# Performance work log

Measured on AMD Instinct MI355X. Metric: run time of the kernel, lower is better.

Reference implementation:

```python
import jax, jax.numpy as jnp
import numpy as np

RATIO = 0.6
ROT_FACTOR = 0.1  # fraction of 2*pi
B, H, W, C = 32, 512, 512, 3
S = 2 * max(H, W)  # mask side = 2*max(H, W) = 1024
FILL_VALUE = 1  # source references undefined self.fill_value; stripes are set to 1


def setup_inputs() -> dict:
    key = jax.random.key(0)
    k1, k2 = jax.random.split(key)
    images = jax.random.uniform(k1, (B, H, W, C), jnp.float32) * 255.0
    max_ang = ROT_FACTOR * 2.0 * np.pi
    angles = jax.random.uniform(k2, (B,), jnp.float32, -max_ang, max_ang)
    rng = np.random.default_rng(0)
    lo = int(min(H * 0.5, W * 0.3))
    hi = int(max(H * 0.5, W * 0.3))
    gridblock = rng.integers(lo, hi + 1, size=B).astype(np.int32)
    start1 = rng.integers(0, gridblock + 1).astype(np.int32)  # uniform [0, gridblock]
    start2 = rng.integers(0, gridblock + 1).astype(np.int32)
    return {
        "images": images,
        "angles": angles,
        "gridblock": jnp.asarray(gridblock),
        "start1": jnp.asarray(start1),
        "start2": jnp.asarray(start2),
    }


def _build_masks(gridblock, start1, start2):
    # Vectorized equivalent of the nested scatter loops: mask[i,j] = 1 iff
    # row i is in a stripe (pass 1) OR column j is in a stripe (pass 2).
    gb = gridblock[:, None].astype(jnp.int32)  # [B,1]
    length = jnp.clip((gb.astype(jnp.float32) * RATIO + 0.5).astype(jnp.int32), 1, gb - 1)
    n = S // gb  # number of stripes per image
    r = jnp.arange(S, dtype=jnp.int32)[None, :]  # [1,S]

    def stripes(start):
        d = r - start[:, None]
        return (d >= 0) & (jnp.mod(d, gb) < length) & ((d // gb) < n)

    rows = stripes(start1)  # [B,S]
    cols = stripes(start2)  # [B,S]
    return (rows[:, :, None] | cols[:, None, :]).astype(jnp.float32)  # [B,S,S]


def _rotate_bilinear_reflect(mask, angles):
    # Rotate each mask about its center by angles[b] (CCW), bilinear interp,
    # reflect fill (TF 'reflect': d c b a | a b c d | d c b a).
    c = (S - 1) / 2.0
    yy, xx = jnp.meshgrid(jnp.arange(S, dtype=jnp.float32),
                          jnp.arange(S, dtype=jnp.float32), indexing="ij")
    cos = jnp.cos(angles)[:, None, None]
    sin = jnp.sin(angles)[:, None, None]
    x = xx[None] - c
    y = yy[None] - c
    sx = cos * x + sin * y + c  # inverse-map source coords [B,S,S]
    sy = -sin * x + cos * y + c
    x0 = jnp.floor(sx)
    y0 = jnp.floor(sy)
    fx = sx - x0
    fy = sy - y0
    x0i = x0.astype(jnp.int32)
    y0i = y0.astype(jnp.int32)

    def refl(i):
        m = jnp.mod(i, 2 * S)
        return jnp.where(m < S, m, 2 * S - 1 - m)

    x0r, x1r = refl(x0i), refl(x0i + 1)
    y0r, y1r = refl(y0i), refl(y0i + 1)
    b = jnp.arange(mask.shape[0])[:, None, None]
    v00 = mask[b, y0r, x0r]
    v01 = mask[b, y0r, x1r]
    v10 = mask[b, y1r, x0r]
    v11 = mask[b, y1r, x1r]
    return (v00 * (1 - fx) * (1 - fy) + v01 * fx * (1 - fy)
            + v10 * (1 - fx) * fy + v11 * fx * fy)


def reference(images, angles, gridblock, start1, start2):
    mask = _build_masks(gridblock, start1, start2) * FILL_VALUE  # [B,S,S]
    rot = _rotate_bilinear_reflect(mask, angles)
    off_h = (S - H) // 2
    off_w = (S - W) // 2
    m = rot[:, off_h:off_h + H, off_w:off_w + W]  # center crop [B,H,W]
    return images * m[..., None]
```

## Files before the change

### kernel.cpp

```cpp
#include <hip/hip_runtime.h>

namespace {
constexpr int S = 1024;
constexpr int H = 512;
constexpr int W = 512;
constexpr int B = 32;
constexpr int OFF = 256;

__device__ __forceinline__ int refl(int i) {
    int m = i & (2 * S - 1);
    return (m < S) ? m : (2 * S - 1 - m);
}

__device__ __forceinline__ bool stripe(int i, int start, int gb, int len, int n, float inv_gb) {
    int d = i - start;
    if (d < 0) return false;
    int q = (int)((float)d * inv_gb);
    int r = d - q * gb;
    if (r < 0)        { r += gb; --q; }
    else if (r >= gb) { r -= gb; ++q; }
    return (r < len) && (q < n);
}

__global__ __launch_bounds__(256) void gridmask_kernel(
    const float* __restrict__ images,
    const float* __restrict__ angles,
    const int* __restrict__ gridblock,
    const int* __restrict__ start1,
    const int* __restrict__ start2,
    float* __restrict__ out)
{
    const int t   = blockIdx.x * 256 + threadIdx.x;
    const int b   = t >> 16;
    const int rem = t & 65535;
    const int y   = rem >> 7;
    const int x   = (rem & 127) << 2;

    const float ang = angles[b];
    const int gb = gridblock[b];
    const int s1 = start1[b];
    const int s2 = start2[b];

    const float gbf = (float)gb;
    int len = (int)(__fadd_rn(__fmul_rn(gbf, 0.6f), 0.5f));
    len = min(max(len, 1), gb - 1);
    const int n = S / gb;
    const float inv_gb = 1.0f / gbf;

    float sn, cs;
    sincosf(ang, &sn, &cs);

    const float c = (float)(S - 1) * 0.5f;
    const float Y = (float)(y + OFF) - c;

    const size_t base = (size_t)t * 12;
    const float4* ip = (const float4*)(images + base);
    const float4 p0 = ip[0];
    const float4 p1 = ip[1];
    const float4 p2 = ip[2];

    float m[4];
#pragma unroll
    for (int i = 0; i < 4; ++i) {
        const float X  = (float)(x + i + OFF) - c;
        const float sx =  cs * X + sn * Y + c;
        const float sy =  cs * Y - sn * X + c;
        const float x0f = floorf(sx);
        const float y0f = floorf(sy);
        const float fx = sx - x0f;
        const float fy = sy - y0f;
        const int x0i = (int)x0f;
        const int y0i = (int)y0f;
        const int x0r = refl(x0i), x1r = refl(x0i + 1);
        const int y0r = refl(y0i), y1r = refl(y0i + 1);
        const bool c0 = stripe(x0r, s2, gb, len, n, inv_gb);
        const bool c1 = stripe(x1r, s2, gb, len, n, inv_gb);
        const bool r0 = stripe(y0r, s1, gb, len, n, inv_gb);
        const bool r1 = stripe(y1r, s1, gb, len, n, inv_gb);
        const float v00 = (r0 | c0) ? 1.0f : 0.0f;
        const float v01 = (r0 | c1) ? 1.0f : 0.0f;
        const float v10 = (r1 | c0) ? 1.0f : 0.0f;
        const float v11 = (r1 | c1) ? 1.0f : 0.0f;
        m[i] = (v00 * (1.0f - fx) + v01 * fx) * (1.0f - fy)
             + (v10 * (1.0f - fx) + v11 * fx) * fy;
    }

    float4 o0, o1, o2;
    o0.x = p0.x * m[0]; o0.y = p0.y * m[0]; o0.z = p0.z * m[0]; o0.w = p0.w * m[1];
    o1.x = p1.x * m[1]; o1.y = p1.y * m[1]; o1.z = p1.z * m[2]; o1.w = p1.w * m[2];
    o2.x = p2.x * m[2]; o2.y = p2.y * m[3]; o2.z = p2.z * m[3]; o2.w = p2.w * m[3];

    float4* op = (float4*)(out + base);
    op[0] = o0; op[1] = o1; op[2] = o2;
}
}

extern "C" void kernel_launch(void* const* d_in, const int* in_sizes, int n_in,
                              void* d_out, int out_size, void* d_ws, size_t ws_size,
                              hipStream_t stream) {
    const float* images    = (const float*)d_in[0];
    const float* angles    = (const float*)d_in[1];
    const int*   gridblock = (const int*)d_in[2];
    const int*   start1    = (const int*)d_in[3];
    const int*   start2    = (const int*)d_in[4];
    float* outp = (float*)d_out;

    const int total_groups = B * H * W / 4;
    const int blocks = total_groups / 256;
    gridmask_kernel<<<blocks, 256, 0, stream>>>(images, angles, gridblock, start1, start2, outp);
}
```

Baseline: 183.7 us.

## Stage mask values in LDS to coalesce image loads and stores

Each block now handles 1024 pixels. It first computes the rotated mask values into shared memory, then reads and writes the image as fully coalesced float4 streams, with consecutive threads touching consecutive float4s. Each thread picks the right mask value from LDS through a divide-by-3 index. Before, each thread loaded 3 strided float4s spaced 48 bytes apart; the new pattern gives contiguous wavefront accesses, at the cost of a barrier and LDS traffic.

```diff
diff --git a/kernel.cpp b/kernel.cpp
--- a/kernel.cpp
+++ b/kernel.cpp
@@ -30,68 +30,93 @@
     const int* __restrict__ start2,
     float* __restrict__ out)
 {
-    const int t   = blockIdx.x * 256 + threadIdx.x;
-    const int b   = t >> 16;
-    const int rem = t & 65535;
-    const int y   = rem >> 7;
-    const int x   = (rem & 127) << 2;
+    __shared__ float mlds[1024];
 
-    const float ang = angles[b];
-    const int gb = gridblock[b];
-    const int s1 = start1[b];
-    const int s2 = start2[b];
+    const int tid = threadIdx.x;
+    const int blk = blockIdx.x;
+    const int b   = blk >> 8;
+    const int pix_base = (blk & 255) << 10;
 
-    const float gbf = (float)gb;
-    int len = (int)(__fadd_rn(__fmul_rn(gbf, 0.6f), 0.5f));
-    len = min(max(len, 1), gb - 1);
-    const int n = S / gb;
-    const float inv_gb = 1.0f / gbf;
+    {
+        const int p0   = tid << 2;
+        const int gpix = pix_base + p0;
+        const int y    = gpix >> 9;
+        const int x    = gpix & 511;
 
-    float sn, cs;
-    sincosf(ang, &sn, &cs);
+        const float ang = angles[b];
+        const int gb = gridblock[b];
+        const int s1 = start1[b];
+        const int s2 = start2[b];
 
-    const float c = (float)(S - 1) * 0.5f;
-    const float Y = (float)(y + OFF) - c;
+        const float gbf = (float)gb;
+        int len = (int)(__fadd_rn(__fmul_rn(gbf, 0.6f), 0.5f));
+        len = min(max(len, 1), gb - 1);
+        const int n = S / gb;
+        const float inv_gb = 1.0f / gbf;
 
-    const size_t base = (size_t)t * 12;
-    const float4* ip = (const float4*)(images + base);
-    const float4 p0 = ip[0];
-    const float4 p1 = ip[1];
-    const float4 p2 = ip[2];
+        float sn, cs;
+        sincosf(ang, &sn, &cs);
 
-    float m[4];
+        const float c = (float)(S - 1) * 0.5f;
+        const float Y = (float)(y + OFF) - c;
+
+        float m[4];
 #pragma unroll
-    for (int i = 0; i < 4; ++i) {
-        const float X  = (float)(x + i + OFF) - c;
-        const float sx =  cs * X + sn * Y + c;
-        const float sy =  cs * Y - sn * X + c;
-        const float x0f = floorf(sx);
-        const float y0f = floorf(sy);
-        const float fx = sx - x0f;
-        const float fy = sy - y0f;
-        const int x0i = (int)x0f;
-        const int y0i = (int)y0f;
-        const int x0r = refl(x0i), x1r = refl(x0i + 1);
-        const int y0r = refl(y0i), y1r = refl(y0i + 1);
-        const bool c0 = stripe(x0r, s2, gb, len, n, inv_gb);
-        const bool c1 = stripe(x1r, s2, gb, len, n, inv_gb);
-        const bool r0 = stripe(y0r, s1, gb, len, n, inv_gb);
-        const bool r1 = stripe(y1r, s1, gb, len, n, inv_gb);
-        const float v00 = (r0 | c0) ? 1.0f : 0.0f;
-        const float v01 = (r0 | c1) ? 1.0f : 0.0f;
-        const float v10 = (r1 | c0) ? 1.0f : 0.0f;
-        const float v11 = (r1 | c1) ? 1.0f : 0.0f;
-        m[i] = (v00 * (1.0f - fx) + v01 * fx) * (1.0f - fy)
-             + (v10 * (1.0f - fx) + v11 * fx) * fy;
+        for (int i = 0; i < 4; ++i) {
+            const float X  = (float)(x + i + OFF) - c;
+            const float sx =  cs * X + sn * Y + c;
+            const float sy =  cs * Y - sn * X + c;
+            const float x0f = floorf(sx);
+            const float y0f = floorf(sy);
+            const float fx = sx - x0f;
+            const float fy = sy - y0f;
+            const int x0i = (int)x0f;
+            const int y0i = (int)y0f;
+            const int x0r = refl(x0i), x1r = refl(x0i + 1);
+            const int y0r = refl(y0i), y1r = refl(y0i + 1);
+            const bool c0 = stripe(x0r, s2, gb, len, n, inv_gb);
+            const bool c1 = stripe(x1r, s2, gb, len, n, inv_gb);
+            const bool r0 = stripe(y0r, s1, gb, len, n, inv_gb);
+            const bool r1 = stripe(y1r, s1, gb, len, n, inv_gb);
+            const float v00 = (r0 | c0) ? 1.0f : 0.0f;
+            const float v01 = (r0 | c1) ? 1.0f : 0.0f;
+            const float v10 = (r1 | c0) ? 1.0f : 0.0f;
+            const float v11 = (r1 | c1) ? 1.0f : 0.0f;
+            m[i] = (v00 * (1.0f - fx) + v01 * fx) * (1.0f - fy)
+                 + (v10 * (1.0f - fx) + v11 * fx) * fy;
+        }
+        float4* ml4 = (float4*)mlds;
+        ml4[tid] = make_float4(m[0], m[1], m[2], m[3]);
     }
+    __syncthreads();
 
-    float4 o0, o1, o2;
-    o0.x = p0.x * m[0]; o0.y = p0.y * m[0]; o0.z = p0.z * m[0]; o0.w = p0.w * m[1];
-    o1.x = p1.x * m[1]; o1.y = p1.y * m[1]; o1.z = p1.z * m[2]; o1.w = p1.w * m[2];
-    o2.x = p2.x * m[2]; o2.y = p2.y * m[3]; o2.z = p2.z * m[3]; o2.w = p2.w * m[3];
+    const size_t fbase = (size_t)blk * 3072;
+    const float4* __restrict__ gin4  = (const float4*)(images + fbase);
+    float4* __restrict__       gout4 = (float4*)(out + fbase);
 
-    float4* op = (float4*)(out + base);
-    op[0] = o0; op[1] = o1; op[2] = o2;
+    const float4 p0 = gin4[tid];
+    const float4 p1 = gin4[tid + 256];
+    const float4 p2 = gin4[tid + 512];
+
+#pragma unroll
+    for (int j = 0; j < 3; ++j) {
+        const int lf = (j << 10) + (tid << 2);
+        const int q  = lf / 3;
+        const int r  = lf - q * 3;
+        const float ma = mlds[q];
+        const float mb = mlds[q + 1 <= 1023 ? q + 1 : 1023];
+        const float m0 = (r + 0 >= 3) ? mb : ma;
+        const float m1 = (r + 1 >= 3) ? mb : ma;
+        const float m2 = (r + 2 >= 3) ? mb : ma;
+        const float m3 = (r + 3 >= 3) ? mb : ma;
+        const float4 p = (j == 0) ? p0 : (j == 1) ? p1 : p2;
+        float4 o;
+        o.x = p.x * m0;
+        o.y = p.y * m1;
+        o.z = p.z * m2;
+        o.w = p.w * m3;
+        gout4[(j << 8) + tid] = o;
+    }
 }
 }
 
@@ -105,7 +130,6 @@
     const int*   start2    = (const int*)d_in[4];
     float* outp = (float*)d_out;
 
-    const int total_groups = B * H * W / 4;
-    const int blocks = total_groups / 256;
+    const int blocks = B * H * W / 1024;
     gridmask_kernel<<<blocks, 256, 0, stream>>>(images, angles, gridblock, start1, start2, outp);
 }
```

After: 181.7 us. About the same (-1.1%).

## Precompute per-image stripe tables in LDS and process 16 pixels per thread

Applied to the files above, without the earlier changes.

Each block now handles 4096 pixels of one image. It precomputes row and column stripe indicator tables in shared memory, and each thread prefetches all 12 float4 image loads up front before computing. The bilinear mask is evaluated with an algebraic identity (ry + cx - ry*cx) using table lookups, which replaces four integer stripe divisions per pixel. In exchange there is an LDS table build and a __syncthreads per block, plus higher register pressure from holding 12 float4s.

```diff
diff --git a/kernel.cpp b/kernel.cpp
--- a/kernel.cpp
+++ b/kernel.cpp
@@ -30,11 +30,25 @@
     const int* __restrict__ start2,
     float* __restrict__ out)
 {
-    const int t   = blockIdx.x * 256 + threadIdx.x;
-    const int b   = t >> 16;
-    const int rem = t & 65535;
-    const int y   = rem >> 7;
-    const int x   = (rem & 127) << 2;
+    __shared__ float rowt[1024];
+    __shared__ float colt[1024];
+
+    const int tid = threadIdx.x;
+    const int blk = blockIdx.x;
+    const int b   = blk >> 6;
+    const int pix_base = (blk & 63) << 12;
+
+    const size_t fbase = (size_t)blk * 12288;
+    const float4* __restrict__ gin4  = (const float4*)(images + fbase);
+    float4* __restrict__       gout4 = (float4*)(out + fbase);
+
+    float4 px[12];
+#pragma unroll
+    for (int g = 0; g < 4; ++g) {
+        const int v4 = (g << 8) * 3 + tid * 3;
+#pragma unroll
+        for (int j = 0; j < 3; ++j) px[g * 3 + j] = gin4[v4 + j];
+    }
 
     const float ang = angles[b];
     const int gb = gridblock[b];
@@ -47,51 +61,61 @@
     const int n = S / gb;
     const float inv_gb = 1.0f / gbf;
 
+    const int i0 = tid << 2;
+#pragma unroll
+    for (int k = 0; k < 4; ++k) {
+        rowt[i0 + k] = stripe(i0 + k, s1, gb, len, n, inv_gb) ? 1.0f : 0.0f;
+        colt[i0 + k] = stripe(i0 + k, s2, gb, len, n, inv_gb) ? 1.0f : 0.0f;
+    }
+
     float sn, cs;
     sincosf(ang, &sn, &cs);
+    const float c = (float)(S - 1) * 0.5f;
 
-    const float c = (float)(S - 1) * 0.5f;
-    const float Y = (float)(y + OFF) - c;
+    __syncthreads();
 
-    const size_t base = (size_t)t * 12;
-    const float4* ip = (const float4*)(images + base);
-    const float4 p0 = ip[0];
-    const float4 p1 = ip[1];
-    const float4 p2 = ip[2];
+#pragma unroll
+    for (int g = 0; g < 4; ++g) {
+        const int lp   = (g << 10) + (tid << 2);
+        const int gpix = pix_base + lp;
+        const int y    = gpix >> 9;
+        const int x    = gpix & 511;
 
-    float m[4];
+        const float Y = (float)(y + OFF) - c;
+        float m[4];
 #pragma unroll
-    for (int i = 0; i < 4; ++i) {
-        const float X  = (float)(x + i + OFF) - c;
-        const float sx =  cs * X + sn * Y + c;
-        const float sy =  cs * Y - sn * X + c;
-        const float x0f = floorf(sx);
-        const float y0f = floorf(sy);
-        const float fx = sx - x0f;
-        const float fy = sy - y0f;
-        const int x0i = (int)x0f;
-        const int y0i = (int)y0f;
-        const int x0r = refl(x0i), x1r = refl(x0i + 1);
-        const int y0r = refl(y0i), y1r = refl(y0i + 1);
-        const bool c0 = stripe(x0r, s2, gb, len, n, inv_gb);
-        const bool c1 = stripe(x1r, s2, gb, len, n, inv_gb);
-        const bool r0 = stripe(y0r, s1, gb, len, n, inv_gb);
-        const bool r1 = stripe(y1r, s1, gb, len, n, inv_gb);
-        const float v00 = (r0 | c0) ? 1.0f : 0.0f;
-        const float v01 = (r0 | c1) ? 1.0f : 0.0f;
-        const float v10 = (r1 | c0) ? 1.0f : 0.0f;
-        const float v11 = (r1 | c1) ? 1.0f : 0.0f;
-        m[i] = (v00 * (1.0f - fx) + v01 * fx) * (1.0f - fy)
-             + (v10 * (1.0f - fx) + v11 * fx) * fy;
+        for (int i = 0; i < 4; ++i) {
+            const float X  = (float)(x + i + OFF) - c;
+            const float sx =  cs * X + sn * Y + c;
+            const float sy =  cs * Y - sn * X + c;
+            const float x0f = floorf(sx);
+            const float y0f = floorf(sy);
+            const float fx = sx - x0f;
+            const float fy = sy - y0f;
+            const int x0i = (int)x0f;
+            const int y0i = (int)y0f;
+            const int x0r = refl(x0i), x1r = refl(x0i + 1);
+            const int y0r = refl(y0i), y1r = refl(y0i + 1);
+            const float r0 = rowt[y0r], r1 = rowt[y1r];
+            const float c0 = colt[x0r], c1 = colt[x1r];
+            const float ry = r0 + fy * (r1 - r0);
+            const float cx = c0 + fx * (c1 - c0);
+            m[i] = ry + cx - ry * cx;
+        }
+
+        const float4 p0 = px[g * 3 + 0];
+        const float4 p1 = px[g * 3 + 1];
+        const float4 p2 = px[g * 3 + 2];
+        float4 o0, o1, o2;
+        o0.x = p0.x * m[0]; o0.y = p0.y * m[0]; o0.z = p0.z * m[0]; o0.w = p0.w * m[1];
+        o1.x = p1.x * m[1]; o1.y = p1.y * m[1]; o1.z = p1.z * m[2]; o1.w = p1.w * m[2];
+        o2.x = p2.x * m[2]; o2.y = p2.y * m[3]; o2.z = p2.z * m[3]; o2.w = p2.w * m[3];
+
+        const int v4 = (g << 8) * 3 + tid * 3;
+        gout4[v4 + 0] = o0;
+        gout4[v4 + 1] = o1;
+        gout4[v4 + 2] = o2;
     }
-
-    float4 o0, o1, o2;
-    o0.x = p0.x * m[0]; o0.y = p0.y * m[0]; o0.z = p0.z * m[0]; o0.w = p0.w * m[1];
-    o1.x = p1.x * m[1]; o1.y = p1.y * m[1]; o1.z = p1.z * m[2]; o1.w = p1.w * m[2];
-    o2.x = p2.x * m[2]; o2.y = p2.y * m[3]; o2.z = p2.z * m[3]; o2.w = p2.w * m[3];
-
-    float4* op = (float4*)(out + base);
-    op[0] = o0; op[1] = o1; op[2] = o2;
 }
 }
 
@@ -105,7 +129,6 @@
     const int*   start2    = (const int*)d_in[4];
     float* outp = (float*)d_out;
 
-    const int total_groups = B * H * W / 4;
-    const int blocks = total_groups / 256;
+    const int blocks = B * H * W / 4096;
     gridmask_kernel<<<blocks, 256, 0, stream>>>(images, angles, gridblock, start1, start2, outp);
 }
```

After: 186.6 us. About the same (+1.6%).
